# Performance work log

Measured on AMD Instinct MI355X. Metric: run time of the kernel, lower is better.

Reference implementation:

```python
import jax, jax.numpy as jnp
import numpy as np

MASK_RATIO = 0.7  # forward default arg


def setup_inputs() -> dict:
    key = jax.random.key(0)
    k1, k2, k3, k4, k5 = jax.random.split(key, 5)
    B, T, D = 16, 2048, 1024
    s = 1.0 / np.sqrt(D)
    return {
        "x": jax.random.normal(k1, (B, T, D), dtype=jnp.float32),
        "W1": jax.random.normal(k2, (D, D), dtype=jnp.float32) * s,
        "b1": jax.random.normal(k3, (D,), dtype=jnp.float32) * s,
        "w2": jax.random.normal(k4, (D,), dtype=jnp.float32) * s,
        "b2": jax.random.normal(k5, (1,), dtype=jnp.float32) * s,
    }


def reference(x, W1, b1, w2, b2):
    # scores: Linear(D,D) -> tanh -> Linear(D,1) -> squeeze
    h = jnp.tanh(jnp.einsum("btd,ed->bte", x, W1) + b1)        # (B,T,D)
    scores = jnp.einsum("btd,d->bt", h, w2) + b2               # (B,T)
    attention_weights = jax.nn.softmax(scores, axis=1)          # (B,T)

    B, T = scores.shape
    num_mask = int(T * MASK_RATIO)
    # indices of the num_mask lowest-scoring frames per batch row
    order = jnp.argsort(scores, axis=1)                         # ascending
    mask_idx = order[:, :num_mask]                              # (B, num_mask)
    mask = jnp.ones_like(attention_weights)
    mask = mask.at[jnp.arange(B)[:, None], mask_idx].set(0.0)
    masked_attention_weights = attention_weights * mask
    masked_output = x * masked_attention_weights[..., None]
    return masked_output, masked_attention_weights
```

## Files before the change

kernel.cpp:

```cpp
#include <hip/hip_runtime.h>
#include <cmath>

constexpr int BATCH  = 16;
constexpr int T      = 2048;
constexpr int D      = 1024;
constexpr int NTOK   = BATCH * T;
constexpr int NUM_MASK = 1433;
constexpr int PCOLS  = 8;

typedef __attribute__((ext_vector_type(8))) short short8;
typedef __attribute__((ext_vector_type(4))) float f32x4;

static __device__ __forceinline__ unsigned short bf16_rne(float f) {
  unsigned int u = __float_as_uint(f);
  u += 0x7fffu + ((u >> 16) & 1u);
  return (unsigned short)(u >> 16);
}
static __device__ __forceinline__ float bf16_to_f(unsigned short h) {
  return __uint_as_float(((unsigned int)h) << 16);
}
static __device__ __forceinline__ void cvt2(float a, float b,
                                            unsigned int& hi, unsigned int& lo) {
  unsigned short ha = bf16_rne(a), hb = bf16_rne(b);
  unsigned short la = bf16_rne(a - bf16_to_f(ha));
  unsigned short lb = bf16_rne(b - bf16_to_f(hb));
  hi = (unsigned int)ha | ((unsigned int)hb << 16);
  lo = (unsigned int)la | ((unsigned int)lb << 16);
}

__global__ __launch_bounds__(256) void k_convW(
    const float4* __restrict__ W1, uint2* __restrict__ Wh, uint2* __restrict__ Wl)
{
  const int i = blockIdx.x * 256 + threadIdx.x;
  const float4 v = W1[i];
  unsigned int h0, l0, h1, l1;
  cvt2(v.x, v.y, h0, l0);
  cvt2(v.z, v.w, h1, l1);
  Wh[i] = make_uint2(h0, h1);
  Wl[i] = make_uint2(l0, l1);
}

#define LDA 40
__global__ __launch_bounds__(256) void k_scores_mfma(
    const float* __restrict__ x, const unsigned short* __restrict__ Wh,
    const unsigned short* __restrict__ Wl, const float* __restrict__ b1,
    const float* __restrict__ w2, float* __restrict__ partial)
{
  __shared__ __align__(16) unsigned short Ah[128 * LDA];
  __shared__ __align__(16) unsigned short Al[128 * LDA];
  __shared__ __align__(16) unsigned short Bh[128 * LDA];
  __shared__ __align__(16) unsigned short Bl[128 * LDA];
  __shared__ float red[128][2];

  const int bx = blockIdx.x;
  const int by = blockIdx.y;
  const int n0 = bx * 128;
  const int m0 = by * 128;
  const int t    = threadIdx.x;
  const int lane = t & 63;
  const int w    = t >> 6;
  const int wm   = (w >> 1) * 64;
  const int wn   = (w & 1) * 64;
  const int c    = lane & 15;
  const int q    = lane >> 4;

  const int r   = t >> 1;
  const int h16 = (t & 1) * 16;

  const float*          aptr  = x  + (size_t)(m0 + r) * D + h16;
  const unsigned short* bhptr = Wh + (size_t)(n0 + r) * D + h16;
  const unsigned short* blptr = Wl + (size_t)(n0 + r) * D + h16;

  f32x4 acc[4][4];
#pragma unroll
  for (int i = 0; i < 4; ++i)
#pragma unroll
    for (int j = 0; j < 4; ++j)
      acc[i][j] = (f32x4){0.f, 0.f, 0.f, 0.f};

  for (int k0 = 0; k0 < D; k0 += 32) {
    const float4 a0 = *(const float4*)(aptr + k0 + 0);
    const float4 a1 = *(const float4*)(aptr + k0 + 4);
    const float4 a2 = *(const float4*)(aptr + k0 + 8);
    const float4 a3 = *(const float4*)(aptr + k0 + 12);
    const uint4 bh0 = *(const uint4*)(bhptr + k0);
    const uint4 bh1 = *(const uint4*)(bhptr + k0 + 8);
    const uint4 bl0 = *(const uint4*)(blptr + k0);
    const uint4 bl1 = *(const uint4*)(blptr + k0 + 8);

    uint4 hA0, lA0, hA1, lA1;
    cvt2(a0.x, a0.y, hA0.x, lA0.x); cvt2(a0.z, a0.w, hA0.y, lA0.y);
    cvt2(a1.x, a1.y, hA0.z, lA0.z); cvt2(a1.z, a1.w, hA0.w, lA0.w);
    cvt2(a2.x, a2.y, hA1.x, lA1.x); cvt2(a2.z, a2.w, hA1.y, lA1.y);
    cvt2(a3.x, a3.y, hA1.z, lA1.z); cvt2(a3.z, a3.w, hA1.w, lA1.w);

    __syncthreads();
    *(uint4*)&Ah[r * LDA + h16]     = hA0;
    *(uint4*)&Ah[r * LDA + h16 + 8] = hA1;
    *(uint4*)&Al[r * LDA + h16]     = lA0;
    *(uint4*)&Al[r * LDA + h16 + 8] = lA1;
    *(uint4*)&Bh[r * LDA + h16]     = bh0;
    *(uint4*)&Bh[r * LDA + h16 + 8] = bh1;
    *(uint4*)&Bl[r * LDA + h16]     = bl0;
    *(uint4*)&Bl[r * LDA + h16 + 8] = bl1;
    __syncthreads();

    short8 avh[4], avl[4], bvh[4], bvl[4];
#pragma unroll
    for (int i = 0; i < 4; ++i) {
      const int ar = (wm + i * 16 + c) * LDA + q * 8;
      const int br = (wn + i * 16 + c) * LDA + q * 8;
      avh[i] = *(const short8*)&Ah[ar];
      avl[i] = *(const short8*)&Al[ar];
      bvh[i] = *(const short8*)&Bh[br];
      bvl[i] = *(const short8*)&Bl[br];
    }
#pragma unroll
    for (int i = 0; i < 4; ++i)
#pragma unroll
      for (int j = 0; j < 4; ++j)
        acc[i][j] = __builtin_amdgcn_mfma_f32_16x16x32_bf16(avh[i], bvh[j], acc[i][j], 0, 0, 0);
#pragma unroll
    for (int i = 0; i < 4; ++i)
#pragma unroll
      for (int j = 0; j < 4; ++j)
        acc[i][j] = __builtin_amdgcn_mfma_f32_16x16x32_bf16(avl[i], bvh[j], acc[i][j], 0, 0, 0);
#pragma unroll
    for (int i = 0; i < 4; ++i)
#pragma unroll
      for (int j = 0; j < 4; ++j)
        acc[i][j] = __builtin_amdgcn_mfma_f32_16x16x32_bf16(avh[i], bvl[j], acc[i][j], 0, 0, 0);
  }

  float b1v[4], w2v[4];
#pragma unroll
  for (int j = 0; j < 4; ++j) {
    const int n = n0 + wn + j * 16 + c;
    b1v[j] = b1[n];
    w2v[j] = w2[n];
  }
  float rs[4][4];
#pragma unroll
  for (int i = 0; i < 4; ++i)
#pragma unroll
    for (int rr = 0; rr < 4; ++rr) {
      float s = 0.f;
#pragma unroll
      for (int j = 0; j < 4; ++j) {
        const float z = acc[i][j][rr] + b1v[j];
        const float th = 1.f - 2.f / (__expf(2.f * z) + 1.f);
        s += th * w2v[j];
      }
      rs[i][rr] = s;
    }
#pragma unroll
  for (int off = 1; off < 16; off <<= 1)
#pragma unroll
    for (int i = 0; i < 4; ++i)
#pragma unroll
      for (int rr = 0; rr < 4; ++rr)
        rs[i][rr] += __shfl_xor(rs[i][rr], off);
  if (c == 0) {
#pragma unroll
    for (int i = 0; i < 4; ++i)
#pragma unroll
      for (int rr = 0; rr < 4; ++rr)
        red[wm + i * 16 + q * 4 + rr][w & 1] = rs[i][rr];
  }
  __syncthreads();
  if (t < 128)
    partial[(size_t)(m0 + t) * PCOLS + bx] = red[t][0] + red[t][1];
}

__global__ __launch_bounds__(256) void k_softmax(
    const float* __restrict__ partial, const float* __restrict__ b2,
    float* __restrict__ s_buf, float* __restrict__ w_buf)
{
  const int b = blockIdx.x;
  const int t = threadIdx.x;
  __shared__ __align__(16) float s[T];
  __shared__ float red[8];

  const float b2v = b2[0];
  for (int i = t; i < T; i += 256) {
    const float* p = partial + (size_t)(b * T + i) * PCOLS;
    float a = 0.f;
#pragma unroll
    for (int j = 0; j < PCOLS; ++j) a += p[j];
    const float v = a + b2v;
    s[i] = v;
    s_buf[b * T + i] = v;
  }
  __syncthreads();

  float m = -INFINITY;
  for (int i = t; i < T; i += 256) m = fmaxf(m, s[i]);
  for (int off = 32; off > 0; off >>= 1) m = fmaxf(m, __shfl_down(m, off));
  if ((t & 63) == 0) red[t >> 6] = m;
  __syncthreads();
  if (t == 0) {
    float mm = -INFINITY;
    for (int i = 0; i < 4; ++i) mm = fmaxf(mm, red[i]);
    red[4] = mm;
  }
  __syncthreads();
  m = red[4];
  __syncthreads();

  float zs = 0.f;
  for (int i = t; i < T; i += 256) zs += expf(s[i] - m);
  for (int off = 32; off > 0; off >>= 1) zs += __shfl_down(zs, off);
  if ((t & 63) == 0) red[t >> 6] = zs;
  __syncthreads();
  if (t == 0) {
    float zz = 0.f;
    for (int i = 0; i < 4; ++i) zz += red[i];
    red[5] = zz;
  }
  __syncthreads();
  const float Z = red[5];

  for (int i = t; i < T; i += 256) w_buf[b * T + i] = expf(s[i] - m) / Z;
}

__global__ __launch_bounds__(256) void k_mask(
    const float* __restrict__ s_buf, const float* __restrict__ w_buf,
    float* __restrict__ mw, float* __restrict__ out_w)
{
  const int b  = blockIdx.y;
  const int i0 = blockIdx.x * 256;
  const int t  = threadIdx.x;
  __shared__ __align__(16) float s[T];
  for (int i = t; i < T; i += 256) s[i] = s_buf[b * T + i];
  __syncthreads();

  const int i = i0 + t;
  const float si = s[i];
  int r = 0;
  const float4* s4 = (const float4*)s;
#pragma unroll 4
  for (int j4 = 0; j4 < T / 4; ++j4) {
    const float4 v = s4[j4];
    const int jb = j4 * 4;
    r += (v.x < si) || ((v.x == si) && (jb + 0 < i));
    r += (v.y < si) || ((v.y == si) && (jb + 1 < i));
    r += (v.z < si) || ((v.z == si) && (jb + 2 < i));
    r += (v.w < si) || ((v.w == si) && (jb + 3 < i));
  }
  const float v = (r < NUM_MASK) ? 0.f : w_buf[b * T + i];
  mw[b * T + i]    = v;
  out_w[b * T + i] = v;
}

__global__ __launch_bounds__(256) void k_output(
    const float4* __restrict__ x4, const float* __restrict__ mw,
    float4* __restrict__ out4)
{
  const int n4 = NTOK * (D / 4);
  int idx = blockIdx.x * blockDim.x + threadIdx.x;
  const int stride = gridDim.x * blockDim.x;
  for (; idx < n4; idx += stride) {
    float4 v = x4[idx];
    const float wv = mw[idx >> 8];
    v.x *= wv; v.y *= wv; v.z *= wv; v.w *= wv;
    out4[idx] = v;
  }
}

extern "C" void kernel_launch(void* const* d_in, const int* in_sizes, int n_in,
                              void* d_out, int out_size, void* d_ws, size_t ws_size,
                              hipStream_t stream) {
  const float* x  = (const float*)d_in[0];
  const float* W1 = (const float*)d_in[1];
  const float* b1 = (const float*)d_in[2];
  const float* w2 = (const float*)d_in[3];
  const float* b2 = (const float*)d_in[4];
  float* out = (float*)d_out;

  unsigned short* Wh = (unsigned short*)d_ws;
  unsigned short* Wl = Wh + (size_t)D * D;
  float* partial = (float*)(Wl + (size_t)D * D);
  float* s_buf   = partial + (size_t)NTOK * PCOLS;
  float* w_buf   = s_buf + NTOK;
  float* mw      = w_buf + NTOK;

  hipLaunchKernelGGL(k_convW, dim3((D * D / 4) / 256), dim3(256), 0, stream,
                     (const float4*)W1, (uint2*)Wh, (uint2*)Wl);
  hipLaunchKernelGGL(k_scores_mfma, dim3(8, NTOK / 128), dim3(256), 0, stream,
                     x, Wh, Wl, b1, w2, partial);
  hipLaunchKernelGGL(k_softmax, dim3(BATCH), dim3(256), 0, stream, partial, b2, s_buf, w_buf);
  hipLaunchKernelGGL(k_mask, dim3(T / 256, BATCH), dim3(256), 0, stream,
                     s_buf, w_buf, mw, out + (size_t)NTOK * D);
  hipLaunchKernelGGL(k_output, dim3(8192), dim3(256), 0, stream,
                     (const float4*)x, mw, (float4*)out);
}
```

Baseline: 547.4 us.

## Prepack W in MFMA fragment layout, DMA it to LDS, fuse softmax and mask

W1 halves are now stored pre-tiled in per-lane MFMA fragment order. This lets the GEMM load B tiles straight into LDS with global_load_lds, skipping the register round trip, and lets the A tile use a fragment-ordered LDS layout without padding. The softmax and rank-mask kernels are merged into one 1024-thread block per batch row, removing intermediate s/w buffers and a launch. The cost is that the fused kernel runs only 16 blocks, each doing the O(T^2) rank counting, so the mask stage has very low parallelism. The new LDS layout may also cause bank conflicts.

```diff
diff --git a/kernel.cpp b/kernel.cpp
--- a/kernel.cpp
+++ b/kernel.cpp
@@ -28,28 +28,40 @@
   lo = (unsigned int)la | ((unsigned int)lb << 16);
 }
 
+static __device__ __forceinline__ void dma16(const void* g, void* l) {
+  __builtin_amdgcn_global_load_lds(
+      (const __attribute__((address_space(1))) void*)g,
+      (__attribute__((address_space(3))) void*)l, 16, 0, 0);
+}
+
 __global__ __launch_bounds__(256) void k_convW(
-    const float4* __restrict__ W1, uint2* __restrict__ Wh, uint2* __restrict__ Wl)
-{
-  const int i = blockIdx.x * 256 + threadIdx.x;
-  const float4 v = W1[i];
-  unsigned int h0, l0, h1, l1;
-  cvt2(v.x, v.y, h0, l0);
-  cvt2(v.z, v.w, h1, l1);
-  Wh[i] = make_uint2(h0, h1);
-  Wl[i] = make_uint2(l0, l1);
-}
-
-#define LDA 40
+    const float* __restrict__ W1, uint4* __restrict__ Whp, uint4* __restrict__ Wlp)
+{
+  const int tid = blockIdx.x * 256 + threadIdx.x;
+  const int l  = tid & 63;
+  const int kt = (tid >> 6) & 31;
+  const int g  = tid >> 11;
+  const int row = g * 16 + (l & 15);
+  const int k   = kt * 32 + (l >> 4) * 8;
+  const float4 f0 = *(const float4*)(W1 + (size_t)row * D + k);
+  const float4 f1 = *(const float4*)(W1 + (size_t)row * D + k + 4);
+  uint4 h, lo;
+  cvt2(f0.x, f0.y, h.x, lo.x); cvt2(f0.z, f0.w, h.y, lo.y);
+  cvt2(f1.x, f1.y, h.z, lo.z); cvt2(f1.z, f1.w, h.w, lo.w);
+  Whp[tid] = h;
+  Wlp[tid] = lo;
+}
+
 __global__ __launch_bounds__(256) void k_scores_mfma(
-    const float* __restrict__ x, const unsigned short* __restrict__ Wh,
-    const unsigned short* __restrict__ Wl, const float* __restrict__ b1,
-    const float* __restrict__ w2, float* __restrict__ partial)
-{
-  __shared__ __align__(16) unsigned short Ah[128 * LDA];
-  __shared__ __align__(16) unsigned short Al[128 * LDA];
-  __shared__ __align__(16) unsigned short Bh[128 * LDA];
-  __shared__ __align__(16) unsigned short Bl[128 * LDA];
+    const float* __restrict__ x,
+    const unsigned short* __restrict__ Whp, const unsigned short* __restrict__ Wlp,
+    const float* __restrict__ b1, const float* __restrict__ w2,
+    float* __restrict__ partial)
+{
+  __shared__ __align__(16) unsigned short Ah[8 * 512];
+  __shared__ __align__(16) unsigned short Al[8 * 512];
+  __shared__ __align__(16) unsigned short Bh[8 * 512];
+  __shared__ __align__(16) unsigned short Bl[8 * 512];
   __shared__ float red[128][2];
 
   const int bx = blockIdx.x;
@@ -64,12 +76,18 @@
   const int c    = lane & 15;
   const int q    = lane >> 4;
 
-  const int r   = t >> 1;
-  const int h16 = (t & 1) * 16;
-
-  const float*          aptr  = x  + (size_t)(m0 + r) * D + h16;
-  const unsigned short* bhptr = Wh + (size_t)(n0 + r) * D + h16;
-  const unsigned short* blptr = Wl + (size_t)(n0 + r) * D + h16;
+  const int r  = t >> 1;
+  const int hh = t & 1;
+  const int cA = r & 15, gA = r >> 4;
+  const float* aptr = x + (size_t)(m0 + r) * D + hh * 16;
+  const int wo0 = gA * 512 + ((2 * hh) * 16 + cA) * 8;
+  const int wo1 = gA * 512 + ((2 * hh + 1) * 16 + cA) * 8;
+
+  const int ch0 = 2 * w, ch1 = 2 * w + 1;
+  const char* whB = (const char*)Whp;
+  const char* wlB = (const char*)Wlp;
+  const size_t bb0 = ((size_t)(n0 / 16 + ch0) * 32) * 1024 + lane * 16;
+  const size_t bb1 = ((size_t)(n0 / 16 + ch1) * 32) * 1024 + lane * 16;
 
   f32x4 acc[4][4];
 #pragma unroll
@@ -78,42 +96,35 @@
     for (int j = 0; j < 4; ++j)
       acc[i][j] = (f32x4){0.f, 0.f, 0.f, 0.f};
 
-  for (int k0 = 0; k0 < D; k0 += 32) {
-    const float4 a0 = *(const float4*)(aptr + k0 + 0);
-    const float4 a1 = *(const float4*)(aptr + k0 + 4);
-    const float4 a2 = *(const float4*)(aptr + k0 + 8);
-    const float4 a3 = *(const float4*)(aptr + k0 + 12);
-    const uint4 bh0 = *(const uint4*)(bhptr + k0);
-    const uint4 bh1 = *(const uint4*)(bhptr + k0 + 8);
-    const uint4 bl0 = *(const uint4*)(blptr + k0);
-    const uint4 bl1 = *(const uint4*)(blptr + k0 + 8);
-
-    uint4 hA0, lA0, hA1, lA1;
-    cvt2(a0.x, a0.y, hA0.x, lA0.x); cvt2(a0.z, a0.w, hA0.y, lA0.y);
-    cvt2(a1.x, a1.y, hA0.z, lA0.z); cvt2(a1.z, a1.w, hA0.w, lA0.w);
-    cvt2(a2.x, a2.y, hA1.x, lA1.x); cvt2(a2.z, a2.w, hA1.y, lA1.y);
-    cvt2(a3.x, a3.y, hA1.z, lA1.z); cvt2(a3.z, a3.w, hA1.w, lA1.w);
+  for (int kt = 0; kt < 32; ++kt) {
+    const float4 f0 = *(const float4*)(aptr + kt * 32 + 0);
+    const float4 f1 = *(const float4*)(aptr + kt * 32 + 4);
+    const float4 f2 = *(const float4*)(aptr + kt * 32 + 8);
+    const float4 f3 = *(const float4*)(aptr + kt * 32 + 12);
+    uint4 h0, l0, h1, l1;
+    cvt2(f0.x, f0.y, h0.x, l0.x); cvt2(f0.z, f0.w, h0.y, l0.y);
+    cvt2(f1.x, f1.y, h0.z, l0.z); cvt2(f1.z, f1.w, h0.w, l0.w);
+    cvt2(f2.x, f2.y, h1.x, l1.x); cvt2(f2.z, f2.w, h1.y, l1.y);
+    cvt2(f3.x, f3.y, h1.z, l1.z); cvt2(f3.z, f3.w, h1.w, l1.w);
 
     __syncthreads();
-    *(uint4*)&Ah[r * LDA + h16]     = hA0;
-    *(uint4*)&Ah[r * LDA + h16 + 8] = hA1;
-    *(uint4*)&Al[r * LDA + h16]     = lA0;
-    *(uint4*)&Al[r * LDA + h16 + 8] = lA1;
-    *(uint4*)&Bh[r * LDA + h16]     = bh0;
-    *(uint4*)&Bh[r * LDA + h16 + 8] = bh1;
-    *(uint4*)&Bl[r * LDA + h16]     = bl0;
-    *(uint4*)&Bl[r * LDA + h16 + 8] = bl1;
+    *(uint4*)&Ah[wo0] = h0;  *(uint4*)&Ah[wo1] = h1;
+    *(uint4*)&Al[wo0] = l0;  *(uint4*)&Al[wo1] = l1;
+    dma16(whB + bb0 + kt * 1024, &Bh[ch0 * 512]);
+    dma16(whB + bb1 + kt * 1024, &Bh[ch1 * 512]);
+    dma16(wlB + bb0 + kt * 1024, &Bl[ch0 * 512]);
+    dma16(wlB + bb1 + kt * 1024, &Bl[ch1 * 512]);
     __syncthreads();
 
     short8 avh[4], avl[4], bvh[4], bvl[4];
 #pragma unroll
     for (int i = 0; i < 4; ++i) {
-      const int ar = (wm + i * 16 + c) * LDA + q * 8;
-      const int br = (wn + i * 16 + c) * LDA + q * 8;
-      avh[i] = *(const short8*)&Ah[ar];
-      avl[i] = *(const short8*)&Al[ar];
-      bvh[i] = *(const short8*)&Bh[br];
-      bvl[i] = *(const short8*)&Bl[br];
+      const int ao = ((wm >> 4) + i) * 512 + lane * 8;
+      const int bo = ((wn >> 4) + i) * 512 + lane * 8;
+      avh[i] = *(const short8*)&Ah[ao];
+      avl[i] = *(const short8*)&Al[ao];
+      bvh[i] = *(const short8*)&Bh[bo];
+      bvl[i] = *(const short8*)&Bl[bo];
     }
 #pragma unroll
     for (int i = 0; i < 4; ++i)
@@ -172,84 +183,69 @@
     partial[(size_t)(m0 + t) * PCOLS + bx] = red[t][0] + red[t][1];
 }
 
-__global__ __launch_bounds__(256) void k_softmax(
+__global__ __launch_bounds__(1024) void k_softmax_mask(
     const float* __restrict__ partial, const float* __restrict__ b2,
-    float* __restrict__ s_buf, float* __restrict__ w_buf)
+    float* __restrict__ mw, float* __restrict__ out_w)
 {
   const int b = blockIdx.x;
   const int t = threadIdx.x;
   __shared__ __align__(16) float s[T];
-  __shared__ float red[8];
+  __shared__ float red[18];
 
   const float b2v = b2[0];
-  for (int i = t; i < T; i += 256) {
+  for (int i = t; i < T; i += 1024) {
     const float* p = partial + (size_t)(b * T + i) * PCOLS;
     float a = 0.f;
 #pragma unroll
     for (int j = 0; j < PCOLS; ++j) a += p[j];
-    const float v = a + b2v;
-    s[i] = v;
-    s_buf[b * T + i] = v;
-  }
-  __syncthreads();
-
-  float m = -INFINITY;
-  for (int i = t; i < T; i += 256) m = fmaxf(m, s[i]);
+    s[i] = a + b2v;
+  }
+  __syncthreads();
+
+  const int wid = t >> 6, ln = t & 63;
+  float m = fmaxf(s[t], s[t + 1024]);
   for (int off = 32; off > 0; off >>= 1) m = fmaxf(m, __shfl_down(m, off));
-  if ((t & 63) == 0) red[t >> 6] = m;
+  if (ln == 0) red[wid] = m;
   __syncthreads();
   if (t == 0) {
-    float mm = -INFINITY;
-    for (int i = 0; i < 4; ++i) mm = fmaxf(mm, red[i]);
-    red[4] = mm;
-  }
-  __syncthreads();
-  m = red[4];
-  __syncthreads();
-
-  float zs = 0.f;
-  for (int i = t; i < T; i += 256) zs += expf(s[i] - m);
+    float mm = red[0];
+    for (int i = 1; i < 16; ++i) mm = fmaxf(mm, red[i]);
+    red[16] = mm;
+  }
+  __syncthreads();
+  const float M = red[16];
+
+  float zs = expf(s[t] - M) + expf(s[t + 1024] - M);
   for (int off = 32; off > 0; off >>= 1) zs += __shfl_down(zs, off);
-  if ((t & 63) == 0) red[t >> 6] = zs;
+  if (ln == 0) red[wid] = zs;
   __syncthreads();
   if (t == 0) {
     float zz = 0.f;
-    for (int i = 0; i < 4; ++i) zz += red[i];
-    red[5] = zz;
-  }
-  __syncthreads();
-  const float Z = red[5];
-
-  for (int i = t; i < T; i += 256) w_buf[b * T + i] = expf(s[i] - m) / Z;
-}
-
-__global__ __launch_bounds__(256) void k_mask(
-    const float* __restrict__ s_buf, const float* __restrict__ w_buf,
-    float* __restrict__ mw, float* __restrict__ out_w)
-{
-  const int b  = blockIdx.y;
-  const int i0 = blockIdx.x * 256;
-  const int t  = threadIdx.x;
-  __shared__ __align__(16) float s[T];
-  for (int i = t; i < T; i += 256) s[i] = s_buf[b * T + i];
-  __syncthreads();
-
-  const int i = i0 + t;
-  const float si = s[i];
-  int r = 0;
+    for (int i = 0; i < 16; ++i) zz += red[i];
+    red[17] = zz;
+  }
+  __syncthreads();
+  const float Z = red[17];
+
   const float4* s4 = (const float4*)s;
+#pragma unroll
+  for (int ii = 0; ii < 2; ++ii) {
+    const int i = t + ii * 1024;
+    const float si = s[i];
+    int r = 0;
 #pragma unroll 4
-  for (int j4 = 0; j4 < T / 4; ++j4) {
-    const float4 v = s4[j4];
-    const int jb = j4 * 4;
-    r += (v.x < si) || ((v.x == si) && (jb + 0 < i));
-    r += (v.y < si) || ((v.y == si) && (jb + 1 < i));
-    r += (v.z < si) || ((v.z == si) && (jb + 2 < i));
-    r += (v.w < si) || ((v.w == si) && (jb + 3 < i));
-  }
-  const float v = (r < NUM_MASK) ? 0.f : w_buf[b * T + i];
-  mw[b * T + i]    = v;
-  out_w[b * T + i] = v;
+    for (int j4 = 0; j4 < T / 4; ++j4) {
+      const float4 v = s4[j4];
+      const int jb = j4 * 4;
+      r += (v.x < si) || ((v.x == si) && (jb + 0 < i));
+      r += (v.y < si) || ((v.y == si) && (jb + 1 < i));
+      r += (v.z < si) || ((v.z == si) && (jb + 2 < i));
+      r += (v.w < si) || ((v.w == si) && (jb + 3 < i));
+    }
+    const float wv = (r < NUM_MASK) ? 0.f : expf(si - M) / Z;
+    mw[b * T + i]    = wv;
+    out_w[b * T + i] = wv;
+  }
 }
 
 __global__ __launch_bounds__(256) void k_output(
@@ -277,20 +273,17 @@
   const float* b2 = (const float*)d_in[4];
   float* out = (float*)d_out;
 
-  unsigned short* Wh = (unsigned short*)d_ws;
-  unsigned short* Wl = Wh + (size_t)D * D;
-  float* partial = (float*)(Wl + (size_t)D * D);
-  float* s_buf   = partial + (size_t)NTOK * PCOLS;
-  float* w_buf   = s_buf + NTOK;
-  float* mw      = w_buf + NTOK;
-
-  hipLaunchKernelGGL(k_convW, dim3((D * D / 4) / 256), dim3(256), 0, stream,
-                     (const float4*)W1, (uint2*)Wh, (uint2*)Wl);
+  unsigned short* Whp = (unsigned short*)d_ws;
+  unsigned short* Wlp = Whp + (size_t)D * D;
+  float* partial = (float*)(Wlp + (size_t)D * D);
+  float* mw      = partial + (size_t)NTOK * PCOLS;
+
+  hipLaunchKernelGGL(k_convW, dim3((D * D / 8) / 256), dim3(256), 0, stream,
+                     W1, (uint4*)Whp, (uint4*)Wlp);
   hipLaunchKernelGGL(k_scores_mfma, dim3(8, NTOK / 128), dim3(256), 0, stream,
-                     x, Wh, Wl, b1, w2, partial);
-  hipLaunchKernelGGL(k_softmax, dim3(BATCH), dim3(256), 0, stream, partial, b2, s_buf, w_buf);
-  hipLaunchKernelGGL(k_mask, dim3(T / 256, BATCH), dim3(256), 0, stream,
-                     s_buf, w_buf, mw, out + (size_t)NTOK * D);
+                     x, Whp, Wlp, b1, w2, partial);
+  hipLaunchKernelGGL(k_softmax_mask, dim3(BATCH), dim3(1024), 0, stream,
+                     partial, b2, mw, out + (size_t)NTOK * D);
   hipLaunchKernelGGL(k_output, dim3(8192), dim3(256), 0, stream,
                      (const float4*)x, mw, (float4*)out);
 }
```

Result: slower. 640.0 us (+16.9%).
